# Kernel optimization log

Hardware: AMD Instinct MI355X
Metric: run time of the kernel (lower is better)

The kernel has to match this reference:

```python
import jax, jax.numpy as jnp
import numpy as np

IN_CH, OUT_CH, HEAD, QK_DIM, V_DIM = 256, 256, 8, 512, 512


def setup_inputs() -> dict:
    key = jax.random.key(0)
    ks = jax.random.split(key, 5)
    B, H, W = 16, 32, 32
    x = jax.random.normal(ks[0], (B, IN_CH, H, W), dtype=jnp.float32)
    # 1x1 conv weights stored as [out_ch, in_ch]
    qkv_out = 2 * QK_DIM + V_DIM
    qkv_w = jax.random.normal(ks[1], (qkv_out, IN_CH), dtype=jnp.float32) * (IN_CH ** -0.5)
    qkv_b = jax.random.normal(ks[2], (qkv_out,), dtype=jnp.float32) * 0.02
    proj_w = jax.random.normal(ks[3], (OUT_CH, V_DIM), dtype=jnp.float32) * (V_DIM ** -0.5)
    proj_b = jax.random.normal(ks[4], (OUT_CH,), dtype=jnp.float32) * 0.02
    return {"x": x, "qkv_w": qkv_w, "qkv_b": qkv_b, "proj_w": proj_w, "proj_b": proj_b}


def reference(x, qkv_w, qkv_b, proj_w, proj_b):
    B, C, H, W = x.shape
    N = H * W
    dh = QK_DIM // HEAD
    dv = V_DIM // HEAD
    scale = dh ** -0.5
    # 1x1 conv == channel GEMM
    qkv = jnp.einsum('bchw,oc->bohw', x, qkv_w) + qkv_b[None, :, None, None]
    q, k, v = jnp.split(qkv, [QK_DIM, 2 * QK_DIM], axis=1)
    # [B, ch, H, W] -> [B, head, N, head_dim]
    def to_heads(t, d):
        return t.reshape(B, HEAD, d, N).transpose(0, 1, 3, 2)
    q = to_heads(q, dh)
    k = to_heads(k, dh)
    v = to_heads(v, dv)
    mask = jnp.tril(jnp.ones((N, N), dtype=bool))  # [N, N]
    scores = jnp.einsum('bhnd,bhmd->bhnm', q, k) * scale
    scores = jnp.where(mask, scores, -jnp.inf)
    attn = jax.nn.softmax(scores, axis=-1)
    attn = jnp.where(mask, attn, 0.0)
    out = jnp.einsum('bhnm,bhmd->bhnd', attn, v)  # [B, head, N, dv]
    out = out.transpose(0, 1, 3, 2).reshape(B, V_DIM, H, W)
    out = jnp.einsum('bvhw,ov->bohw', out, proj_w) + proj_b[None, :, None, None]
    return out
```

## Files before the change

kernel.cpp:

```cpp
#include <hip/hip_runtime.h>
#include <math.h>

static constexpr int Bsz = 16;
static constexpr int Np  = 1024;
static constexpr int Cin = 256;

typedef __attribute__((ext_vector_type(8))) short short8;
typedef __attribute__((ext_vector_type(4))) float f4;

#if defined(__has_builtin)
#if __has_builtin(__builtin_amdgcn_exp2f)
#define EXP2(x) __builtin_amdgcn_exp2f(x)
#else
#define EXP2(x) exp2f(x)
#endif
#else
#define EXP2(x) exp2f(x)
#endif

#define QSCALE 0.18033688011112f

__device__ __forceinline__ unsigned short f2b(float f) {
    union { float fp; unsigned int u; } v; v.fp = f;
    unsigned int r = v.u + 0x7fffu + ((v.u >> 16) & 1u);
    return (unsigned short)(r >> 16);
}

__global__ __launch_bounds__(256)
void cast_xw(const float* __restrict__ x, const float* __restrict__ qw,
             const float* __restrict__ pw, ushort* __restrict__ xb,
             ushort* __restrict__ qwb, ushort* __restrict__ pwb)
{
    const int t = threadIdx.x;
    if (blockIdx.y < 4) {
        __shared__ ushort T[64][72];
        const int n0 = blockIdx.x * 64, c0 = blockIdx.y * 64, b = blockIdx.z;
        {
            const int c_l = t >> 2, ns = (t & 3) * 16;
            const float* src = &x[((b * Cin + c0 + c_l) << 10) + n0 + ns];
#pragma unroll
            for (int i = 0; i < 4; ++i) {
                const float4 v = *(const float4*)(src + 4 * i);
                T[ns + 4 * i + 0][c_l] = f2b(v.x);
                T[ns + 4 * i + 1][c_l] = f2b(v.y);
                T[ns + 4 * i + 2][c_l] = f2b(v.z);
                T[ns + 4 * i + 3][c_l] = f2b(v.w);
            }
        }
        __syncthreads();
        {
            const int n_l = t >> 2, cs = (t & 3) * 16;
            ushort* dst = &xb[((b << 10) + n0 + n_l) * Cin + c0 + cs];
            *(uint4*)dst       = *(const uint4*)&T[n_l][cs];
            *(uint4*)(dst + 8) = *(const uint4*)&T[n_l][cs + 8];
        }
    } else {
        const int nq4 = (1536 * Cin) / 4;
        const int base = ((blockIdx.z * 16 + blockIdx.x) * 256 + t) * 2;
#pragma unroll
        for (int g = 0; g < 2; ++g) {
            const int j = base + g;
            const float* src; ushort* dst; int jj;
            if (j < nq4) { src = qw; dst = qwb; jj = j; }
            else         { src = pw; dst = pwb; jj = j - nq4; }
            const float4 v = *(const float4*)(src + 4 * jj);
            ushort4 u; u.x = f2b(v.x); u.y = f2b(v.y); u.z = f2b(v.z); u.w = f2b(v.w);
            *(ushort4*)(dst + 4 * jj) = u;
        }
    }
}

__global__ __launch_bounds__(256)
void qkv_gemm(const ushort* __restrict__ xb, const ushort* __restrict__ wb,
              const float* __restrict__ bias,
              ushort* __restrict__ qb, ushort* __restrict__ kb, ushort* __restrict__ vb)
{
    __shared__ ushort lds[18432];
    ushort* As = lds;
    ushort* Bs = lds + 9216;

    const int t = threadIdx.x;
    const int w = t >> 6, lane = t & 63, quad = lane >> 4, ln = lane & 15;
    const int n0 = blockIdx.x * 128;
    const int o0 = blockIdx.y * 128;
    const int b  = blockIdx.z;
    const int ow = (w & 1) * 64, nw = (w >> 1) * 64;
    const bool vpath = (o0 >= 1024);

    f4 acc[4][4];
#pragma unroll
    for (int i = 0; i < 4; ++i)
#pragma unroll
        for (int j = 0; j < 4; ++j) acc[i][j] = (f4){0.f, 0.f, 0.f, 0.f};

    const int rr = t >> 2, cc = (t & 3) * 16;
    for (int k0 = 0; k0 < Cin; k0 += 64) {
        __syncthreads();
#pragma unroll
        for (int p = 0; p < 2; ++p) {
            const int row = rr + p * 64;
            const ushort* sa = &wb[(o0 + row) * Cin + k0 + cc];
            *(uint4*)&As[row * 72 + cc]     = *(const uint4*)sa;
            *(uint4*)&As[row * 72 + cc + 8] = *(const uint4*)(sa + 8);
            const ushort* sb = &xb[((b << 10) + n0 + row) * Cin + k0 + cc];
            *(uint4*)&Bs[row * 72 + cc]     = *(const uint4*)sb;
            *(uint4*)&Bs[row * 72 + cc + 8] = *(const uint4*)(sb + 8);
        }
        __syncthreads();
#pragma unroll
        for (int sub = 0; sub < 2; ++sub) {
            short8 af[4], bf[4];
#pragma unroll
            for (int ot = 0; ot < 4; ++ot)
                af[ot] = *(const short8*)&As[(ow + ot * 16 + ln) * 72 + sub * 32 + quad * 8];
#pragma unroll
            for (int nt = 0; nt < 4; ++nt)
                bf[nt] = *(const short8*)&Bs[(nw + nt * 16 + ln) * 72 + sub * 32 + quad * 8];
            if (!vpath) {
#pragma unroll
                for (int ot = 0; ot < 4; ++ot)
#pragma unroll
                    for (int nt = 0; nt < 4; ++nt)
                        acc[ot][nt] = __builtin_amdgcn_mfma_f32_16x16x32_bf16(
                            af[ot], bf[nt], acc[ot][nt], 0, 0, 0);
            } else {
#pragma unroll
                for (int nt = 0; nt < 4; ++nt)
#pragma unroll
                    for (int ot = 0; ot < 4; ++ot)
                        acc[nt][ot] = __builtin_amdgcn_mfma_f32_16x16x32_bf16(
                            bf[nt], af[ot], acc[nt][ot], 0, 0, 0);
            }
        }
    }

    __syncthreads();
    if (!vpath) {
        ushort* Ct = lds;
        const float sc = (o0 < 512) ? QSCALE : 1.0f;
#pragma unroll
        for (int ot = 0; ot < 4; ++ot) {
            float bs[4];
#pragma unroll
            for (int rg = 0; rg < 4; ++rg)
                bs[rg] = bias[o0 + ow + ot * 16 + quad * 4 + rg];
#pragma unroll
            for (int nt = 0; nt < 4; ++nt) {
                ushort4 u;
                u.x = f2b((acc[ot][nt][0] + bs[0]) * sc);
                u.y = f2b((acc[ot][nt][1] + bs[1]) * sc);
                u.z = f2b((acc[ot][nt][2] + bs[2]) * sc);
                u.w = f2b((acc[ot][nt][3] + bs[3]) * sc);
                *(ushort4*)&Ct[(nw + nt * 16 + ln) * 136 + ow + ot * 16 + quad * 4] = u;
            }
        }
        __syncthreads();
        ushort* dst; int obase;
        if (o0 < 512) { dst = qb; obase = o0; }
        else          { dst = kb; obase = o0 - 512; }
        const int rn = t >> 1, hf = t & 1;
        const int bh = b * 8 + (obase >> 6) + hf;
        ushort* drow = &dst[(bh * Np + n0 + rn) << 6];
        const ushort* srow = &Ct[rn * 136 + hf * 64];
#pragma unroll
        for (int s = 0; s < 8; ++s)
            *(uint4*)(drow + s * 8) = *(const uint4*)(srow + s * 8);
    } else {
        ushort* Ct = lds;
#pragma unroll
        for (int ot = 0; ot < 4; ++ot) {
            const float bo = bias[o0 + ow + ot * 16 + ln];
#pragma unroll
            for (int nt = 0; nt < 4; ++nt) {
                ushort4 u;
                u.x = f2b(acc[nt][ot][0] + bo);
                u.y = f2b(acc[nt][ot][1] + bo);
                u.z = f2b(acc[nt][ot][2] + bo);
                u.w = f2b(acc[nt][ot][3] + bo);
                *(ushort4*)&Ct[(ow + ot * 16 + ln) * 136 + nw + nt * 16 + quad * 4] = u;
            }
        }
        __syncthreads();
        const int o_l = t >> 1, nh = (t & 1) * 64;
        const int bh = b * 8 + ((o0 - 1024) >> 6) + (o_l >> 6);
        ushort* drow = &vb[((size_t)bh << 16) + ((o_l & 63) << 10) + n0 + nh];
        const ushort* srow = &Ct[o_l * 136 + nh];
#pragma unroll
        for (int s = 0; s < 8; ++s)
            *(uint4*)(drow + s * 8) = *(const uint4*)(srow + s * 8);
    }
}

__global__ __launch_bounds__(256, 4)
void attn(const ushort* __restrict__ qb, const ushort* __restrict__ kb,
          const ushort* __restrict__ vt, ushort* __restrict__ ob)
{
    __shared__ ushort Qs[64 * 72];
    __shared__ ushort Ks[64 * 72];
    __shared__ ushort Vt[64 * 72];
    __shared__ ushort Ps[64 * 72];

    const int t    = threadIdx.x;
    const int w    = t >> 6;
    const int lane = t & 63;
    const int quad = lane >> 4;
    const int ln   = lane & 15;
    const int bh   = blockIdx.x & 127;
    const int qt   = 15 - (blockIdx.x >> 7);
    const int q0   = qt * 64;

    {
        const int r = t & 63, seg = t >> 6;
        const ushort* src = &qb[((bh * Np + q0 + r) << 6) + seg * 16];
        *(uint4*)&Qs[r * 72 + seg * 16]     = *(const uint4*)src;
        *(uint4*)&Qs[r * 72 + seg * 16 + 8] = *(const uint4*)(src + 8);
    }
    __syncthreads();

    const short8 qa0 = *(const short8*)&Qs[(w * 16 + ln) * 72 + quad * 8];
    const short8 qa1 = *(const short8*)&Qs[(w * 16 + ln) * 72 + 32 + quad * 8];

    f4 o_[4];
#pragma unroll
    for (int nt = 0; nt < 4; ++nt) o_[nt] = (f4){0.f, 0.f, 0.f, 0.f};
    float mrun = -INFINITY, lrun = 0.f;

    for (int kt = 0; kt <= qt; ++kt) {
        __syncthreads();
        {
            const int r = t & 63, seg = t >> 6;
            const ushort* sk = &kb[((bh * Np + kt * 64 + r) << 6) + seg * 16];
            *(uint4*)&Ks[r * 72 + seg * 16]     = *(const uint4*)sk;
            *(uint4*)&Ks[r * 72 + seg * 16 + 8] = *(const uint4*)(sk + 8);
            const int dd = t >> 2, c = (t & 3) * 16;
            const ushort* sv = &vt[((size_t)bh << 16) + (dd << 10) + kt * 64 + c];
            *(uint4*)&Vt[dd * 72 + c]     = *(const uint4*)sv;
            *(uint4*)&Vt[dd * 72 + c + 8] = *(const uint4*)(sv + 8);
        }
        __syncthreads();

        const bool diag = (kt == qt);

        f4 st[4];
#pragma unroll
        for (int mt = 0; mt < 4; ++mt) st[mt] = (f4){0.f, 0.f, 0.f, 0.f};
#pragma unroll
        for (int mt = 0; mt < 4; ++mt) {
            if (diag && mt > w) continue;
            const short8 ka0 = *(const short8*)&Ks[(mt * 16 + ln) * 72 + quad * 8];
            const short8 ka1 = *(const short8*)&Ks[(mt * 16 + ln) * 72 + 32 + quad * 8];
            st[mt] = __builtin_amdgcn_mfma_f32_16x16x32_bf16(ka0, qa0, st[mt], 0, 0, 0);
            st[mt] = __builtin_amdgcn_mfma_f32_16x16x32_bf16(ka1, qa1, st[mt], 0, 0, 0);
        }

        if (diag) {
            const int qrow = w * 16 + ln;
#pragma unroll
            for (int mt = 0; mt < 4; ++mt)
#pragma unroll
                for (int rg = 0; rg < 4; ++rg)
                    if (mt * 16 + quad * 4 + rg > qrow) st[mt][rg] = -INFINITY;
        }

        float mx = -INFINITY;
#pragma unroll
        for (int mt = 0; mt < 4; ++mt)
#pragma unroll
            for (int rg = 0; rg < 4; ++rg) mx = fmaxf(mx, st[mt][rg]);
        mx = fmaxf(mx, __shfl_xor(mx, 16));
        mx = fmaxf(mx, __shfl_xor(mx, 32));

        const float mn = fmaxf(mrun, mx);
        const float al = EXP2(mrun - mn);
        mrun = mn;

        float rs = 0.f;
        const int prow = (w * 16 + ln) * 72;
#pragma unroll
        for (int mt = 0; mt < 4; ++mt) {
            float p0 = EXP2(st[mt][0] - mn), p1 = EXP2(st[mt][1] - mn);
            float p2 = EXP2(st[mt][2] - mn), p3 = EXP2(st[mt][3] - mn);
            rs += (p0 + p1) + (p2 + p3);
            ushort4 u; u.x = f2b(p0); u.y = f2b(p1); u.z = f2b(p2); u.w = f2b(p3);
            *(ushort4*)&Ps[prow + mt * 16 + quad * 4] = u;
        }
        rs += __shfl_xor(rs, 16);
        rs += __shfl_xor(rs, 32);
        lrun = lrun * al + rs;

        float alr[4];
#pragma unroll
        for (int rg = 0; rg < 4; ++rg) alr[rg] = __shfl(al, quad * 4 + rg);
#pragma unroll
        for (int nt = 0; nt < 4; ++nt)
#pragma unroll
            for (int rg = 0; rg < 4; ++rg) o_[nt][rg] *= alr[rg];

#pragma unroll
        for (int ks = 0; ks < 2; ++ks) {
            if (diag && w * 16 + 15 < ks * 32) continue;
            const short8 pa = *(const short8*)&Ps[prow + ks * 32 + quad * 8];
#pragma unroll
            for (int nt = 0; nt < 4; ++nt) {
                const short8 vf = *(const short8*)&Vt[(nt * 16 + ln) * 72 + ks * 32 + quad * 8];
                o_[nt] = __builtin_amdgcn_mfma_f32_16x16x32_bf16(pa, vf, o_[nt], 0, 0, 0);
            }
        }
    }

    const float linv = 1.0f / lrun;
    float lr[4];
#pragma unroll
    for (int rg = 0; rg < 4; ++rg) lr[rg] = __shfl(linv, quad * 4 + rg);
#pragma unroll
    for (int rg = 0; rg < 4; ++rg) {
        const int rr = q0 + w * 16 + quad * 4 + rg;
#pragma unroll
        for (int nt = 0; nt < 4; ++nt)
            ob[((bh * Np + rr) << 6) + nt * 16 + ln] = f2b(o_[nt][rg] * lr[rg]);
    }
}

__global__ __launch_bounds__(256)
void proj_gemm(const ushort* __restrict__ obuf, const ushort* __restrict__ pwb,
               const float* __restrict__ bias, float* __restrict__ out)
{
    __shared__ ushort As[64 * 72];
    __shared__ ushort Bs[128 * 72];

    const int t = threadIdx.x;
    const int w = t >> 6, lane = t & 63, quad = lane >> 4, ln = lane & 15;
    const int n0 = blockIdx.x * 128;
    const int o0 = blockIdx.y * 64;
    const int b  = blockIdx.z;
    const int nw = w * 32;

    f4 acc[4][2];
#pragma unroll
    for (int i = 0; i < 4; ++i)
#pragma unroll
        for (int j = 0; j < 2; ++j) acc[i][j] = (f4){0.f, 0.f, 0.f, 0.f};

    const int rr = t >> 2, cc = (t & 3) * 16;
    for (int k0 = 0; k0 < 512; k0 += 64) {
        __syncthreads();
        {
            const ushort* sa = &pwb[(o0 + rr) * 512 + k0 + cc];
            *(uint4*)&As[rr * 72 + cc]     = *(const uint4*)sa;
            *(uint4*)&As[rr * 72 + cc + 8] = *(const uint4*)(sa + 8);
            const int head = k0 >> 6;
#pragma unroll
            for (int p = 0; p < 2; ++p) {
                const int row = rr + p * 64;
                const ushort* sb = &obuf[(((b * 8 + head) * Np + n0 + row) << 6) + cc];
                *(uint4*)&Bs[row * 72 + cc]     = *(const uint4*)sb;
                *(uint4*)&Bs[row * 72 + cc + 8] = *(const uint4*)(sb + 8);
            }
        }
        __syncthreads();
#pragma unroll
        for (int sub = 0; sub < 2; ++sub) {
            short8 af[4], bf[2];
#pragma unroll
            for (int ot = 0; ot < 4; ++ot)
                af[ot] = *(const short8*)&As[(ot * 16 + ln) * 72 + sub * 32 + quad * 8];
#pragma unroll
            for (int nt = 0; nt < 2; ++nt)
                bf[nt] = *(const short8*)&Bs[(nw + nt * 16 + ln) * 72 + sub * 32 + quad * 8];
#pragma unroll
            for (int ot = 0; ot < 4; ++ot)
#pragma unroll
                for (int nt = 0; nt < 2; ++nt)
                    acc[ot][nt] = __builtin_amdgcn_mfma_f32_16x16x32_bf16(
                        af[ot], bf[nt], acc[ot][nt], 0, 0, 0);
        }
    }

#pragma unroll
    for (int ot = 0; ot < 4; ++ot) {
#pragma unroll
        for (int rg = 0; rg < 4; ++rg) {
            const int oo = o0 + ot * 16 + quad * 4 + rg;
            const float pb = bias[oo];
            float* drow = &out[((b << 8) + oo) << 10];
#pragma unroll
            for (int nt = 0; nt < 2; ++nt)
                drow[n0 + nw + nt * 16 + ln] = acc[ot][nt][rg] + pb;
        }
    }
}

extern "C" void kernel_launch(void* const* d_in, const int* in_sizes, int n_in,
                              void* d_out, int out_size, void* d_ws, size_t ws_size,
                              hipStream_t stream)
{
    const float* x   = (const float*)d_in[0];
    const float* qw  = (const float*)d_in[1];
    const float* qbb = (const float*)d_in[2];
    const float* pw  = (const float*)d_in[3];
    const float* pb  = (const float*)d_in[4];
    float* out = (float*)d_out;

    const size_t per = (size_t)Bsz * 8 * Np * 64;
    ushort* qbuf = (ushort*)d_ws;
    ushort* kbuf = qbuf + per;
    ushort* vbuf = kbuf + per;
    ushort* obuf = vbuf + per;
    ushort* xb   = obuf + per;
    ushort* qwb  = xb + (size_t)Bsz * Np * Cin;
    ushort* pwb  = qwb + 1536 * Cin;

    cast_xw<<<dim3(16, 5, Bsz), 256, 0, stream>>>(x, qw, pw, xb, qwb, pwb);
    qkv_gemm<<<dim3(8, 12, Bsz), 256, 0, stream>>>(xb, qwb, qbb, qbuf, kbuf, vbuf);
    attn<<<dim3(128 * 16), 256, 0, stream>>>(qbuf, kbuf, vbuf, obuf);
    proj_gemm<<<dim3(8, 4, Bsz), 256, 0, stream>>>(obuf, pwb, pb, out);
}
```

Baseline: 164.2 us.

## Restructure causal attention: 128-row Q tiles, direct-global K/V, lazy softmax rescale

The attention kernel now gives each block 128 query rows, and each wave handles two 16-row subtiles so every K/V fragment it loads is reused twice. K and V fragments are read straight from global memory into registers instead of being staged in shared memory, which removes the per-tile block barriers. The online softmax skips rescaling the accumulators unless the row max grows by more than a threshold. Scores are computed transposed so the per-row statistics line up with the output layout without extra shuffles. The change also adds packed bf16 conversion, MFMA priority hints and vectorized output stores; in exchange the kernel uses more registers and relies on cache hits for K/V reuse across waves.

```diff
diff --git a/kernel.cpp b/kernel.cpp
--- a/kernel.cpp
+++ b/kernel.cpp
@@ -24,6 +24,12 @@
     union { float fp; unsigned int u; } v; v.fp = f;
     unsigned int r = v.u + 0x7fffu + ((v.u >> 16) & 1u);
     return (unsigned short)(r >> 16);
+}
+
+__device__ __forceinline__ unsigned cvtpk(float a, float b) {
+    unsigned r;
+    asm("v_cvt_pk_bf16_f32 %0, %1, %2" : "=v"(r) : "v"(a), "v"(b));
+    return r;
 }
 
 __global__ __launch_bounds__(256)
@@ -195,10 +201,7 @@
 void attn(const ushort* __restrict__ qb, const ushort* __restrict__ kb,
           const ushort* __restrict__ vt, ushort* __restrict__ ob)
 {
-    __shared__ ushort Qs[64 * 72];
-    __shared__ ushort Ks[64 * 72];
-    __shared__ ushort Vt[64 * 72];
-    __shared__ ushort Ps[64 * 72];
+    __shared__ ushort Ps[128 * 72];
 
     const int t    = threadIdx.x;
     const int w    = t >> 6;
@@ -206,118 +209,173 @@
     const int quad = lane >> 4;
     const int ln   = lane & 15;
     const int bh   = blockIdx.x & 127;
-    const int qt   = 15 - (blockIdx.x >> 7);
-    const int q0   = qt * 64;
-
+    const int qbk  = 7 - (int)(blockIdx.x >> 7);
+    const int q0   = qbk * 128;
+
+    const int base0 = q0 + w * 32;
+    const int qhi0  = base0 + 15;
+    const int qhi1  = base0 + 31;
+
+    const ushort* __restrict__ kbh = kb + ((size_t)(bh * Np) << 6);
+    const ushort* __restrict__ vbh = vt + ((size_t)bh << 16);
+
+    short8 qa00, qa01, qa10, qa11;
     {
-        const int r = t & 63, seg = t >> 6;
-        const ushort* src = &qb[((bh * Np + q0 + r) << 6) + seg * 16];
-        *(uint4*)&Qs[r * 72 + seg * 16]     = *(const uint4*)src;
-        *(uint4*)&Qs[r * 72 + seg * 16 + 8] = *(const uint4*)(src + 8);
-    }
-    __syncthreads();
-
-    const short8 qa0 = *(const short8*)&Qs[(w * 16 + ln) * 72 + quad * 8];
-    const short8 qa1 = *(const short8*)&Qs[(w * 16 + ln) * 72 + 32 + quad * 8];
-
-    f4 o_[4];
-#pragma unroll
-    for (int nt = 0; nt < 4; ++nt) o_[nt] = (f4){0.f, 0.f, 0.f, 0.f};
-    float mrun = -INFINITY, lrun = 0.f;
-
-    for (int kt = 0; kt <= qt; ++kt) {
-        __syncthreads();
+        const ushort* qr = &qb[((size_t)(bh * Np + base0 + ln) << 6) + quad * 8];
+        qa00 = *(const short8*)qr;
+        qa01 = *(const short8*)(qr + 32);
+        qa10 = *(const short8*)(qr + 1024);
+        qa11 = *(const short8*)(qr + 1024 + 32);
+    }
+
+    f4 o0[4], o1[4];
+#pragma unroll
+    for (int nt = 0; nt < 4; ++nt) { o0[nt] = (f4){0.f,0.f,0.f,0.f}; o1[nt] = (f4){0.f,0.f,0.f,0.f}; }
+    float m0 = -INFINITY, l0 = 0.f;
+    float m1 = -INFINITY, l1 = 0.f;
+
+    const int prow0 = (w * 32 + ln) * 72;
+    const int prow1 = prow0 + 16 * 72;
+
+    const int ktmax = qhi1 >> 6;
+    for (int kt = 0; kt <= ktmax; ++kt) {
+        const int k0 = kt * 64;
+
+        f4 s0[4], s1[4];
+#pragma unroll
+        for (int mt = 0; mt < 4; ++mt) { s0[mt] = (f4){0.f,0.f,0.f,0.f}; s1[mt] = (f4){0.f,0.f,0.f,0.f}; }
+        __builtin_amdgcn_s_setprio(1);
+#pragma unroll
+        for (int mt = 0; mt < 4; ++mt) {
+            const int kmt = k0 + mt * 16;
+            if (kmt > qhi1) continue;
+            const ushort* kr = &kbh[((kmt + ln) << 6) + quad * 8];
+            const short8 ka0 = *(const short8*)kr;
+            const short8 ka1 = *(const short8*)(kr + 32);
+            s1[mt] = __builtin_amdgcn_mfma_f32_16x16x32_bf16(ka0, qa10, s1[mt], 0, 0, 0);
+            s1[mt] = __builtin_amdgcn_mfma_f32_16x16x32_bf16(ka1, qa11, s1[mt], 0, 0, 0);
+            if (kmt <= qhi0) {
+                s0[mt] = __builtin_amdgcn_mfma_f32_16x16x32_bf16(ka0, qa00, s0[mt], 0, 0, 0);
+                s0[mt] = __builtin_amdgcn_mfma_f32_16x16x32_bf16(ka1, qa01, s0[mt], 0, 0, 0);
+            }
+        }
+        __builtin_amdgcn_s_setprio(0);
+
+        if (k0 + 63 > base0) {
+            const int q = base0 + ln;
+#pragma unroll
+            for (int mt = 0; mt < 4; ++mt)
+#pragma unroll
+                for (int rg = 0; rg < 4; ++rg)
+                    if (k0 + mt * 16 + quad * 4 + rg > q) s0[mt][rg] = -INFINITY;
+        }
+        if (k0 + 63 > base0 + 16) {
+            const int q = base0 + 16 + ln;
+#pragma unroll
+            for (int mt = 0; mt < 4; ++mt)
+#pragma unroll
+                for (int rg = 0; rg < 4; ++rg)
+                    if (k0 + mt * 16 + quad * 4 + rg > q) s1[mt][rg] = -INFINITY;
+        }
+
         {
-            const int r = t & 63, seg = t >> 6;
-            const ushort* sk = &kb[((bh * Np + kt * 64 + r) << 6) + seg * 16];
-            *(uint4*)&Ks[r * 72 + seg * 16]     = *(const uint4*)sk;
-            *(uint4*)&Ks[r * 72 + seg * 16 + 8] = *(const uint4*)(sk + 8);
-            const int dd = t >> 2, c = (t & 3) * 16;
-            const ushort* sv = &vt[((size_t)bh << 16) + (dd << 10) + kt * 64 + c];
-            *(uint4*)&Vt[dd * 72 + c]     = *(const uint4*)sv;
-            *(uint4*)&Vt[dd * 72 + c + 8] = *(const uint4*)(sv + 8);
-        }
-        __syncthreads();
-
-        const bool diag = (kt == qt);
-
-        f4 st[4];
-#pragma unroll
-        for (int mt = 0; mt < 4; ++mt) st[mt] = (f4){0.f, 0.f, 0.f, 0.f};
-#pragma unroll
-        for (int mt = 0; mt < 4; ++mt) {
-            if (diag && mt > w) continue;
-            const short8 ka0 = *(const short8*)&Ks[(mt * 16 + ln) * 72 + quad * 8];
-            const short8 ka1 = *(const short8*)&Ks[(mt * 16 + ln) * 72 + 32 + quad * 8];
-            st[mt] = __builtin_amdgcn_mfma_f32_16x16x32_bf16(ka0, qa0, st[mt], 0, 0, 0);
-            st[mt] = __builtin_amdgcn_mfma_f32_16x16x32_bf16(ka1, qa1, st[mt], 0, 0, 0);
-        }
-
-        if (diag) {
-            const int qrow = w * 16 + ln;
+            float mx = s0[0][0];
 #pragma unroll
             for (int mt = 0; mt < 4; ++mt)
 #pragma unroll
-                for (int rg = 0; rg < 4; ++rg)
-                    if (mt * 16 + quad * 4 + rg > qrow) st[mt][rg] = -INFINITY;
-        }
-
-        float mx = -INFINITY;
-#pragma unroll
-        for (int mt = 0; mt < 4; ++mt)
-#pragma unroll
-            for (int rg = 0; rg < 4; ++rg) mx = fmaxf(mx, st[mt][rg]);
-        mx = fmaxf(mx, __shfl_xor(mx, 16));
-        mx = fmaxf(mx, __shfl_xor(mx, 32));
-
-        const float mn = fmaxf(mrun, mx);
-        const float al = EXP2(mrun - mn);
-        mrun = mn;
-
-        float rs = 0.f;
-        const int prow = (w * 16 + ln) * 72;
-#pragma unroll
-        for (int mt = 0; mt < 4; ++mt) {
-            float p0 = EXP2(st[mt][0] - mn), p1 = EXP2(st[mt][1] - mn);
-            float p2 = EXP2(st[mt][2] - mn), p3 = EXP2(st[mt][3] - mn);
-            rs += (p0 + p1) + (p2 + p3);
-            ushort4 u; u.x = f2b(p0); u.y = f2b(p1); u.z = f2b(p2); u.w = f2b(p3);
-            *(ushort4*)&Ps[prow + mt * 16 + quad * 4] = u;
-        }
-        rs += __shfl_xor(rs, 16);
-        rs += __shfl_xor(rs, 32);
-        lrun = lrun * al + rs;
-
-        float alr[4];
-#pragma unroll
-        for (int rg = 0; rg < 4; ++rg) alr[rg] = __shfl(al, quad * 4 + rg);
-#pragma unroll
-        for (int nt = 0; nt < 4; ++nt)
-#pragma unroll
-            for (int rg = 0; rg < 4; ++rg) o_[nt][rg] *= alr[rg];
+                for (int rg = 0; rg < 4; ++rg) mx = fmaxf(mx, s0[mt][rg]);
+            mx = fmaxf(mx, __shfl_xor(mx, 16));
+            mx = fmaxf(mx, __shfl_xor(mx, 32));
+            if (!__all(mx <= m0 + 8.f)) {
+                const float mn = fmaxf(m0, mx);
+                const float al = EXP2(m0 - mn);
+                m0 = mn; l0 *= al;
+#pragma unroll
+                for (int nt = 0; nt < 4; ++nt)
+#pragma unroll
+                    for (int rg = 0; rg < 4; ++rg) o0[nt][rg] *= al;
+            }
+            float rs = 0.f;
+#pragma unroll
+            for (int mt = 0; mt < 4; ++mt) {
+                const float p0 = EXP2(s0[mt][0] - m0);
+                const float p1 = EXP2(s0[mt][1] - m0);
+                const float p2 = EXP2(s0[mt][2] - m0);
+                const float p3 = EXP2(s0[mt][3] - m0);
+                rs += (p0 + p1) + (p2 + p3);
+                uint2 u; u.x = cvtpk(p0, p1); u.y = cvtpk(p2, p3);
+                *(uint2*)&Ps[prow0 + mt * 16 + quad * 4] = u;
+            }
+            rs += __shfl_xor(rs, 16);
+            rs += __shfl_xor(rs, 32);
+            l0 += rs;
+        }
+        {
+            float mx = s1[0][0];
+#pragma unroll
+            for (int mt = 0; mt < 4; ++mt)
+#pragma unroll
+                for (int rg = 0; rg < 4; ++rg) mx = fmaxf(mx, s1[mt][rg]);
+            mx = fmaxf(mx, __shfl_xor(mx, 16));
+            mx = fmaxf(mx, __shfl_xor(mx, 32));
+            if (!__all(mx <= m1 + 8.f)) {
+                const float mn = fmaxf(m1, mx);
+                const float al = EXP2(m1 - mn);
+                m1 = mn; l1 *= al;
+#pragma unroll
+                for (int nt = 0; nt < 4; ++nt)
+#pragma unroll
+                    for (int rg = 0; rg < 4; ++rg) o1[nt][rg] *= al;
+            }
+            float rs = 0.f;
+#pragma unroll
+            for (int mt = 0; mt < 4; ++mt) {
+                const float p0 = EXP2(s1[mt][0] - m1);
+                const float p1 = EXP2(s1[mt][1] - m1);
+                const float p2 = EXP2(s1[mt][2] - m1);
+                const float p3 = EXP2(s1[mt][3] - m1);
+                rs += (p0 + p1) + (p2 + p3);
+                uint2 u; u.x = cvtpk(p0, p1); u.y = cvtpk(p2, p3);
+                *(uint2*)&Ps[prow1 + mt * 16 + quad * 4] = u;
+            }
+            rs += __shfl_xor(rs, 16);
+            rs += __shfl_xor(rs, 32);
+            l1 += rs;
+        }
 
 #pragma unroll
         for (int ks = 0; ks < 2; ++ks) {
-            if (diag && w * 16 + 15 < ks * 32) continue;
-            const short8 pa = *(const short8*)&Ps[prow + ks * 32 + quad * 8];
+            const int kk = k0 + ks * 32;
+            if (kk > qhi1) continue;
+            const short8 pa1 = *(const short8*)&Ps[prow1 + ks * 32 + quad * 8];
+            const short8 pa0 = *(const short8*)&Ps[prow0 + ks * 32 + quad * 8];
+            const bool do0 = (kk <= qhi0);
+            __builtin_amdgcn_s_setprio(1);
 #pragma unroll
             for (int nt = 0; nt < 4; ++nt) {
-                const short8 vf = *(const short8*)&Vt[(nt * 16 + ln) * 72 + ks * 32 + quad * 8];
-                o_[nt] = __builtin_amdgcn_mfma_f32_16x16x32_bf16(pa, vf, o_[nt], 0, 0, 0);
-            }
-        }
-    }
-
-    const float linv = 1.0f / lrun;
-    float lr[4];
-#pragma unroll
-    for (int rg = 0; rg < 4; ++rg) lr[rg] = __shfl(linv, quad * 4 + rg);
-#pragma unroll
-    for (int rg = 0; rg < 4; ++rg) {
-        const int rr = q0 + w * 16 + quad * 4 + rg;
-#pragma unroll
-        for (int nt = 0; nt < 4; ++nt)
-            ob[((bh * Np + rr) << 6) + nt * 16 + ln] = f2b(o_[nt][rg] * lr[rg]);
+                const short8 vf = *(const short8*)&vbh[((nt * 16 + ln) << 10) + kk + quad * 8];
+                o1[nt] = __builtin_amdgcn_mfma_f32_16x16x32_bf16(vf, pa1, o1[nt], 0, 0, 0);
+                if (do0)
+                    o0[nt] = __builtin_amdgcn_mfma_f32_16x16x32_bf16(vf, pa0, o0[nt], 0, 0, 0);
+            }
+            __builtin_amdgcn_s_setprio(0);
+        }
+    }
+
+    const float li0 = 1.0f / l0;
+    const float li1 = 1.0f / l1;
+    ushort* orow0 = &ob[(size_t)(bh * Np + base0 + ln) << 6];
+    ushort* orow1 = orow0 + 1024;
+#pragma unroll
+    for (int nt = 0; nt < 4; ++nt) {
+        uint2 u;
+        u.x = cvtpk(o0[nt][0] * li0, o0[nt][1] * li0);
+        u.y = cvtpk(o0[nt][2] * li0, o0[nt][3] * li0);
+        *(uint2*)(orow0 + nt * 16 + quad * 4) = u;
+        uint2 v;
+        v.x = cvtpk(o1[nt][0] * li1, o1[nt][1] * li1);
+        v.y = cvtpk(o1[nt][2] * li1, o1[nt][3] * li1);
+        *(uint2*)(orow1 + nt * 16 + quad * 4) = v;
     }
 }
 
@@ -412,6 +470,6 @@
 
     cast_xw<<<dim3(16, 5, Bsz), 256, 0, stream>>>(x, qw, pw, xb, qwb, pwb);
     qkv_gemm<<<dim3(8, 12, Bsz), 256, 0, stream>>>(xb, qwb, qbb, qbuf, kbuf, vbuf);
-    attn<<<dim3(128 * 16), 256, 0, stream>>>(qbuf, kbuf, vbuf, obuf);
+    attn<<<dim3(1024), 256, 0, stream>>>(qbuf, kbuf, vbuf, obuf);
     proj_gemm<<<dim3(8, 4, Bsz), 256, 0, stream>>>(obuf, pwb, pb, out);
 }
```

Measured after the change: 197.5 us. 20.3% more time.

## Rework attention inner loop: swizzled LDS, transposed PV, lazy rescale, packed bf16

Applied to the files above, without the earlier changes.

The attention kernel drops the separate Q buffer and stages Q through the P buffer instead, which cuts shared memory and lets the launch bound rise to 6 blocks per SM. K and V tiles now sit in unpadded LDS with an XOR swizzle to avoid bank conflicts. The PV MFMA operands are swapped so each lane holds its own query row, which removes the per-row alpha and 1/l shuffles and allows packed stores of the output. The softmax rescale is skipped unless the running max grows by more than 8 (log2 units), and bf16 conversion uses the v_cvt_pk_bf16_f32 instruction. Together these trade some numeric headroom and register pressure for fewer LDS conflicts, fewer shuffles and higher occupancy.

```diff
diff --git a/kernel.cpp b/kernel.cpp
--- a/kernel.cpp
+++ b/kernel.cpp
@@ -24,6 +24,16 @@
     union { float fp; unsigned int u; } v; v.fp = f;
     unsigned int r = v.u + 0x7fffu + ((v.u >> 16) & 1u);
     return (unsigned short)(r >> 16);
+}
+
+__device__ __forceinline__ unsigned cvtpk(float a, float b) {
+    unsigned r;
+    asm("v_cvt_pk_bf16_f32 %0, %1, %2" : "=v"(r) : "v"(a), "v"(b));
+    return r;
+}
+
+__device__ __forceinline__ void* swzp(const void* base, int row, int col) {
+    return (void*)((const char*)base + ((row * 128 + col * 2) ^ ((row & 7) << 4)));
 }
 
 __global__ __launch_bounds__(256)
@@ -191,13 +201,12 @@
     }
 }
 
-__global__ __launch_bounds__(256, 4)
+__global__ __launch_bounds__(256, 6)
 void attn(const ushort* __restrict__ qb, const ushort* __restrict__ kb,
           const ushort* __restrict__ vt, ushort* __restrict__ ob)
 {
-    __shared__ ushort Qs[64 * 72];
-    __shared__ ushort Ks[64 * 72];
-    __shared__ ushort Vt[64 * 72];
+    __shared__ ushort Ks[64 * 64];
+    __shared__ ushort Vt[64 * 64];
     __shared__ ushort Ps[64 * 72];
 
     const int t    = threadIdx.x;
@@ -206,36 +215,42 @@
     const int quad = lane >> 4;
     const int ln   = lane & 15;
     const int bh   = blockIdx.x & 127;
-    const int qt   = 15 - (blockIdx.x >> 7);
+    const int qt   = 15 - (int)(blockIdx.x >> 7);
     const int q0   = qt * 64;
+
+    const ushort* __restrict__ kbh = kb + ((size_t)(bh * Np) << 6);
+    const ushort* __restrict__ vbh = vt + ((size_t)bh << 16);
 
     {
         const int r = t & 63, seg = t >> 6;
-        const ushort* src = &qb[((bh * Np + q0 + r) << 6) + seg * 16];
-        *(uint4*)&Qs[r * 72 + seg * 16]     = *(const uint4*)src;
-        *(uint4*)&Qs[r * 72 + seg * 16 + 8] = *(const uint4*)(src + 8);
+        const ushort* src = &qb[((size_t)(bh * Np + q0 + r) << 6) + seg * 16];
+        *(uint4*)&Ps[r * 72 + seg * 16]     = *(const uint4*)src;
+        *(uint4*)&Ps[r * 72 + seg * 16 + 8] = *(const uint4*)(src + 8);
     }
     __syncthreads();
 
-    const short8 qa0 = *(const short8*)&Qs[(w * 16 + ln) * 72 + quad * 8];
-    const short8 qa1 = *(const short8*)&Qs[(w * 16 + ln) * 72 + 32 + quad * 8];
+    const short8 qa0 = *(const short8*)&Ps[(w * 16 + ln) * 72 + quad * 8];
+    const short8 qa1 = *(const short8*)&Ps[(w * 16 + ln) * 72 + 32 + quad * 8];
 
     f4 o_[4];
 #pragma unroll
     for (int nt = 0; nt < 4; ++nt) o_[nt] = (f4){0.f, 0.f, 0.f, 0.f};
-    float mrun = -INFINITY, lrun = 0.f;
+    float m = -INFINITY, l = 0.f;
+
+    const int srow = t >> 2, scol = (t & 3) * 16;
+    const int prow = (w * 16 + ln) * 72;
+    const int qrow = q0 + w * 16 + ln;
 
     for (int kt = 0; kt <= qt; ++kt) {
+        const int k0 = kt * 64;
         __syncthreads();
         {
-            const int r = t & 63, seg = t >> 6;
-            const ushort* sk = &kb[((bh * Np + kt * 64 + r) << 6) + seg * 16];
-            *(uint4*)&Ks[r * 72 + seg * 16]     = *(const uint4*)sk;
-            *(uint4*)&Ks[r * 72 + seg * 16 + 8] = *(const uint4*)(sk + 8);
-            const int dd = t >> 2, c = (t & 3) * 16;
-            const ushort* sv = &vt[((size_t)bh << 16) + (dd << 10) + kt * 64 + c];
-            *(uint4*)&Vt[dd * 72 + c]     = *(const uint4*)sv;
-            *(uint4*)&Vt[dd * 72 + c + 8] = *(const uint4*)(sv + 8);
+            const ushort* sk = &kbh[((k0 + srow) << 6) + scol];
+            *(uint4*)swzp(Ks, srow, scol)     = *(const uint4*)sk;
+            *(uint4*)swzp(Ks, srow, scol + 8) = *(const uint4*)(sk + 8);
+            const ushort* sv = &vbh[(srow << 10) + k0 + scol];
+            *(uint4*)swzp(Vt, srow, scol)     = *(const uint4*)sv;
+            *(uint4*)swzp(Vt, srow, scol + 8) = *(const uint4*)(sv + 8);
         }
         __syncthreads();
 
@@ -247,22 +262,21 @@
 #pragma unroll
         for (int mt = 0; mt < 4; ++mt) {
             if (diag && mt > w) continue;
-            const short8 ka0 = *(const short8*)&Ks[(mt * 16 + ln) * 72 + quad * 8];
-            const short8 ka1 = *(const short8*)&Ks[(mt * 16 + ln) * 72 + 32 + quad * 8];
+            const short8 ka0 = *(const short8*)swzp(Ks, mt * 16 + ln, quad * 8);
+            const short8 ka1 = *(const short8*)swzp(Ks, mt * 16 + ln, 32 + quad * 8);
             st[mt] = __builtin_amdgcn_mfma_f32_16x16x32_bf16(ka0, qa0, st[mt], 0, 0, 0);
             st[mt] = __builtin_amdgcn_mfma_f32_16x16x32_bf16(ka1, qa1, st[mt], 0, 0, 0);
         }
 
         if (diag) {
-            const int qrow = w * 16 + ln;
 #pragma unroll
             for (int mt = 0; mt < 4; ++mt)
 #pragma unroll
                 for (int rg = 0; rg < 4; ++rg)
-                    if (mt * 16 + quad * 4 + rg > qrow) st[mt][rg] = -INFINITY;
-        }
-
-        float mx = -INFINITY;
+                    if (k0 + mt * 16 + quad * 4 + rg > qrow) st[mt][rg] = -INFINITY;
+        }
+
+        float mx = st[0][0];
 #pragma unroll
         for (int mt = 0; mt < 4; ++mt)
 #pragma unroll
@@ -270,31 +284,30 @@
         mx = fmaxf(mx, __shfl_xor(mx, 16));
         mx = fmaxf(mx, __shfl_xor(mx, 32));
 
-        const float mn = fmaxf(mrun, mx);
-        const float al = EXP2(mrun - mn);
-        mrun = mn;
+        if (!__all(mx <= m + 8.f)) {
+            const float mn = fmaxf(m, mx);
+            const float al = EXP2(m - mn);
+            m = mn; l *= al;
+#pragma unroll
+            for (int nt = 0; nt < 4; ++nt)
+#pragma unroll
+                for (int rg = 0; rg < 4; ++rg) o_[nt][rg] *= al;
+        }
 
         float rs = 0.f;
-        const int prow = (w * 16 + ln) * 72;
 #pragma unroll
         for (int mt = 0; mt < 4; ++mt) {
-            float p0 = EXP2(st[mt][0] - mn), p1 = EXP2(st[mt][1] - mn);
-            float p2 = EXP2(st[mt][2] - mn), p3 = EXP2(st[mt][3] - mn);
+            const float p0 = EXP2(st[mt][0] - m);
+            const float p1 = EXP2(st[mt][1] - m);
+            const float p2 = EXP2(st[mt][2] - m);
+            const float p3 = EXP2(st[mt][3] - m);
             rs += (p0 + p1) + (p2 + p3);
-            ushort4 u; u.x = f2b(p0); u.y = f2b(p1); u.z = f2b(p2); u.w = f2b(p3);
-            *(ushort4*)&Ps[prow + mt * 16 + quad * 4] = u;
+            uint2 u; u.x = cvtpk(p0, p1); u.y = cvtpk(p2, p3);
+            *(uint2*)&Ps[prow + mt * 16 + quad * 4] = u;
         }
         rs += __shfl_xor(rs, 16);
         rs += __shfl_xor(rs, 32);
-        lrun = lrun * al + rs;
-
-        float alr[4];
-#pragma unroll
-        for (int rg = 0; rg < 4; ++rg) alr[rg] = __shfl(al, quad * 4 + rg);
-#pragma unroll
-        for (int nt = 0; nt < 4; ++nt)
-#pragma unroll
-            for (int rg = 0; rg < 4; ++rg) o_[nt][rg] *= alr[rg];
+        l += rs;
 
 #pragma unroll
         for (int ks = 0; ks < 2; ++ks) {
@@ -302,22 +315,20 @@
             const short8 pa = *(const short8*)&Ps[prow + ks * 32 + quad * 8];
 #pragma unroll
             for (int nt = 0; nt < 4; ++nt) {
-                const short8 vf = *(const short8*)&Vt[(nt * 16 + ln) * 72 + ks * 32 + quad * 8];
-                o_[nt] = __builtin_amdgcn_mfma_f32_16x16x32_bf16(pa, vf, o_[nt], 0, 0, 0);
-            }
-        }
-    }
-
-    const float linv = 1.0f / lrun;
-    float lr[4];
-#pragma unroll
-    for (int rg = 0; rg < 4; ++rg) lr[rg] = __shfl(linv, quad * 4 + rg);
-#pragma unroll
-    for (int rg = 0; rg < 4; ++rg) {
-        const int rr = q0 + w * 16 + quad * 4 + rg;
-#pragma unroll
-        for (int nt = 0; nt < 4; ++nt)
-            ob[((bh * Np + rr) << 6) + nt * 16 + ln] = f2b(o_[nt][rg] * lr[rg]);
+                const short8 vf = *(const short8*)swzp(Vt, nt * 16 + ln, ks * 32 + quad * 8);
+                o_[nt] = __builtin_amdgcn_mfma_f32_16x16x32_bf16(vf, pa, o_[nt], 0, 0, 0);
+            }
+        }
+    }
+
+    const float li = 1.0f / l;
+    ushort* orow = &ob[(size_t)(bh * Np + qrow) << 6];
+#pragma unroll
+    for (int nt = 0; nt < 4; ++nt) {
+        uint2 u;
+        u.x = cvtpk(o_[nt][0] * li, o_[nt][1] * li);
+        u.y = cvtpk(o_[nt][2] * li, o_[nt][3] * li);
+        *(uint2*)(orow + nt * 16 + quad * 4) = u;
     }
 }
 
```

Result: faster. 152.3 us (-7.3%).
